# Kernel optimization log

Hardware: AMD Instinct MI355X
Metric: run time of the kernel (lower is better)

Reference implementation:

```python
import jax, jax.numpy as jnp
import numpy as np

EMBED = 1024
HEADS = 16
HEAD_DIM = EMBED // HEADS
MLP_DIM = 4096
EPS = 1e-5


def setup_inputs() -> dict:
    key = jax.random.key(0)
    ks = jax.random.split(key, 12)
    s = lambda d: 1.0 / np.sqrt(d)
    return {
        "x": jax.random.normal(ks[0], (8, 1024, EMBED), dtype=jnp.float32),
        "ln1_g": jnp.ones((EMBED,), jnp.float32),
        "ln1_b": jnp.zeros((EMBED,), jnp.float32),
        "w_qkv": jax.random.normal(ks[1], (EMBED, 3 * EMBED), jnp.float32) * s(EMBED),
        "b_qkv": jnp.zeros((3 * EMBED,), jnp.float32),
        "w_proj": jax.random.normal(ks[2], (EMBED, EMBED), jnp.float32) * s(EMBED),
        "b_proj": jnp.zeros((EMBED,), jnp.float32),
        "ln2_g": jnp.ones((EMBED,), jnp.float32),
        "ln2_b": jnp.zeros((EMBED,), jnp.float32),
        "w_fc1": jax.random.normal(ks[3], (EMBED, MLP_DIM), jnp.float32) * s(EMBED),
        "b_fc1": jnp.zeros((MLP_DIM,), jnp.float32),
        "w_fc2": jax.random.normal(ks[4], (MLP_DIM, EMBED), jnp.float32) * s(MLP_DIM),
        "b_fc2": jnp.zeros((EMBED,), jnp.float32),
    }


def _layernorm(x, g, b):
    mu = jnp.mean(x, axis=-1, keepdims=True)
    var = jnp.mean(jnp.square(x - mu), axis=-1, keepdims=True)
    return (x - mu) * jax.lax.rsqrt(var + EPS) * g + b


def reference(x, ln1_g, ln1_b, w_qkv, b_qkv, w_proj, b_proj,
              ln2_g, ln2_b, w_fc1, b_fc1, w_fc2, b_fc2):
    B, N, D = x.shape
    scale = HEAD_DIM ** -0.5

    # --- attention branch ---
    h = _layernorm(x, ln1_g, ln1_b)
    qkv = h @ w_qkv + b_qkv                       # [B,N,3D]
    qkv = qkv.reshape(B, N, 3, HEADS, HEAD_DIM)
    q, k, v = jnp.moveaxis(qkv, 2, 0)             # each [B,N,H,hd]
    attn = jnp.einsum('bqhd,bkhd->bhqk', q, k) * scale
    attn = jax.nn.softmax(attn, axis=-1)
    out = jnp.einsum('bhqk,bkhd->bqhd', attn, v).reshape(B, N, D)
    x = x + (out @ w_proj + b_proj)

    # --- MLP branch ---
    h = _layernorm(x, ln2_g, ln2_b)
    h = jax.nn.gelu(h @ w_fc1 + b_fc1, approximate=False)
    x = x + (h @ w_fc2 + b_fc2)
    return x
```

## Files before the change

kernel.cpp:

```cpp
#include <hip/hip_runtime.h>
#include <cstdint>


typedef unsigned short u16;
typedef short short8 __attribute__((ext_vector_type(8)));
typedef float floatx4 __attribute__((ext_vector_type(4)));

#define GLB(p) ((const __attribute__((address_space(1))) void*)(p))
#define LDSP(p) ((__attribute__((address_space(3))) void*)(p))

__device__ __forceinline__ u16 f2bf(float f) {
    uint32_t u = __float_as_uint(f);
    u += 0x7fffu + ((u >> 16) & 1u);
    return (u16)(u >> 16);
}
__device__ __forceinline__ uint32_t pack2(float a, float b) {
    return (uint32_t)f2bf(a) | ((uint32_t)f2bf(b) << 16);
}
__device__ __forceinline__ float fast_gelu(float v) {
    float u = v * (0.7978845608f + 0.0356774081f * v * v);
    float e = __expf(2.0f * u);
    float th = 1.0f - 2.0f * __builtin_amdgcn_rcpf(e + 1.0f);
    return 0.5f * v * (1.0f + th);
}

__global__ __launch_bounds__(256) void transpose_cast_kernel(
    const float* __restrict__ W, u16* __restrict__ Wt, int K, int N)
{
    __shared__ float tile[32][33];
    int n0 = blockIdx.x * 32, k0 = blockIdx.y * 32;
    int tx = threadIdx.x, ty = threadIdx.y;
    #pragma unroll
    for (int i = 0; i < 4; ++i)
        tile[ty + i * 8][tx] = W[(size_t)(k0 + ty + i * 8) * N + n0 + tx];
    __syncthreads();
    #pragma unroll
    for (int i = 0; i < 4; ++i)
        Wt[(size_t)(n0 + ty + i * 8) * K + k0 + tx] = f2bf(tile[tx][ty + i * 8]);
}

__global__ __launch_bounds__(256) void ln_kernel(
    const float* __restrict__ x, const float* __restrict__ gw,
    const float* __restrict__ bw, u16* __restrict__ out)
{
    const int row = blockIdx.x, tid = threadIdx.x;
    float4 v = ((const float4*)(x + (size_t)row * 1024))[tid];
    float s  = v.x + v.y + v.z + v.w;
    float ss = v.x * v.x + v.y * v.y + v.z * v.z + v.w * v.w;
    #pragma unroll
    for (int off = 32; off > 0; off >>= 1) {
        s  += __shfl_down(s, off);
        ss += __shfl_down(ss, off);
    }
    __shared__ float red[8];
    if ((tid & 63) == 0) { red[tid >> 6] = s; red[4 + (tid >> 6)] = ss; }
    __syncthreads();
    float S  = red[0] + red[1] + red[2] + red[3];
    float SS = red[4] + red[5] + red[6] + red[7];
    float mu  = S * (1.0f / 1024.0f);
    float var = SS * (1.0f / 1024.0f) - mu * mu;
    float rs  = rsqrtf(var + 1e-5f);
    float4 g4 = ((const float4*)gw)[tid];
    float4 b4 = ((const float4*)bw)[tid];
    u16* o = out + (size_t)row * 1024 + tid * 4;
    o[0] = f2bf((v.x - mu) * rs * g4.x + b4.x);
    o[1] = f2bf((v.y - mu) * rs * g4.y + b4.y);
    o[2] = f2bf((v.z - mu) * rs * g4.z + b4.z);
    o[3] = f2bf((v.w - mu) * rs * g4.w + b4.w);
}

__global__ __launch_bounds__(256) void add2_kernel(
    const float* __restrict__ a, const float* __restrict__ b,
    float* __restrict__ o, int n4)
{
    int i = blockIdx.x * 256 + threadIdx.x;
    const int stride = gridDim.x * 256;
    for (; i < n4; i += stride) {
        float4 va = ((const float4*)a)[i], vb = ((const float4*)b)[i];
        ((float4*)o)[i] = make_float4(va.x + vb.x, va.y + vb.y, va.z + vb.z, va.w + vb.w);
    }
}

#define MODE_BF16      0
#define MODE_BF16_GELU 1
#define MODE_F32_RES   2
#define MODE_QKV       3
#define MODE_F32_SPLIT 4

#define G8_BUF1 32768
#define G8_LDS_BYTES 131072

#define SB()    __builtin_amdgcn_sched_barrier(0)
#define BARR()  do { __builtin_amdgcn_s_barrier(); SB(); } while (0)
#define GATE4() do { asm volatile("s_waitcnt vmcnt(4)" ::: "memory"); SB(); } while (0)
#define WL0()   do { asm volatile("s_waitcnt lgkmcnt(0)" ::: "memory"); SB(); } while (0)

#define RDA(DST, BUFOFF, MH) \
    _Pragma("unroll") \
    for (int mt = 0; mt < 4; ++mt) \
        _Pragma("unroll") \
        for (int ks = 0; ks < 2; ++ks) \
            DST[mt][ks] = *(const short8*)&lds[(BUFOFF) + \
                (size_t)(wr * 128 + (MH) * 64 + mt * 16 + lc) * 64 + \
                (((ks * 4 + lg) ^ (lc & 7)) * 8)];

#define RDB(DST, BUFOFF, NH) \
    _Pragma("unroll") \
    for (int nn = 0; nn < 2; ++nn) \
        _Pragma("unroll") \
        for (int ks = 0; ks < 2; ++ks) \
            DST[nn][ks] = *(const short8*)&lds[(BUFOFF) + 16384 + \
                (size_t)(wc * 64 + (NH) * 32 + nn * 16 + lc) * 64 + \
                (((ks * 4 + lg) ^ (lc & 7)) * 8)];

#define MMAQ(MH, NH, FA, FB) \
    __builtin_amdgcn_s_setprio(1); \
    _Pragma("unroll") \
    for (int ks = 0; ks < 2; ++ks) \
        _Pragma("unroll") \
        for (int mt = 0; mt < 4; ++mt) \
            _Pragma("unroll") \
            for (int nn = 0; nn < 2; ++nn) \
                acc[(MH) * 4 + mt][(NH) * 2 + nn] = \
                    __builtin_amdgcn_mfma_f32_16x16x32_bf16( \
                        FA[mt][ks], FB[nn][ks], acc[(MH) * 4 + mt][(NH) * 2 + nn], 0, 0, 0); \
    __builtin_amdgcn_s_setprio(0);

template<int MODE>
__global__ __launch_bounds__(512, 2) void gemm8_kernel(
    const u16* __restrict__ A, const u16* __restrict__ Bt,
    const float* __restrict__ bias, const float* __restrict__ res,
    void* __restrict__ outv, u16* __restrict__ vt,
    int M, int N, int lda, int ldb, int K)
{
    extern __shared__ u16 lds[];
    const int tid = threadIdx.x;
    const int wave = tid >> 6, lane = tid & 63;
    const int lg = lane >> 4, lc = lane & 15;
    const int m0 = blockIdx.y * 256, n0 = blockIdx.x * 256;
    const int wr = wave >> 2, wc = wave & 3;
    const int zed = (MODE == MODE_F32_SPLIT) ? blockIdx.z : 0;
    if (MODE == MODE_F32_SPLIT && zed) { A += K; Bt += K; }

    floatx4 acc[8][4];
    #pragma unroll
    for (int i = 0; i < 8; ++i)
        #pragma unroll
        for (int j = 0; j < 4; ++j) acc[i][j] = floatx4{0.f, 0.f, 0.f, 0.f};

    const int srow = lane >> 3;
    const int schunk = (lane & 7) ^ srow;

    const u16* Abase = A  + (size_t)(m0 + wave * 8 + srow) * lda + schunk * 8;
    const u16* Bbase = Bt + (size_t)(n0 + wave * 8 + srow) * ldb + schunk * 8;

    auto stageH = [&](int b, int o, int h, int kk) {
        if (o == 0) {
            const u16* src = Abase + (size_t)h * 128 * lda + kk;
            u16* dst = lds + b * G8_BUF1 + h * 8192 + wave * 512;
            __builtin_amdgcn_global_load_lds(GLB(src), LDSP(dst), 16, 0, 0);
            __builtin_amdgcn_global_load_lds(GLB(src + (size_t)64 * lda), LDSP(dst + 4096), 16, 0, 0);
        } else {
            const u16* src = Bbase + (size_t)h * 128 * ldb + kk;
            u16* dst = lds + b * G8_BUF1 + 16384 + h * 8192 + wave * 512;
            __builtin_amdgcn_global_load_lds(GLB(src), LDSP(dst), 16, 0, 0);
            __builtin_amdgcn_global_load_lds(GLB(src + (size_t)64 * ldb), LDSP(dst + 4096), 16, 0, 0);
        }
    };

    const int nt = K >> 6;

    stageH(0, 0, 0, 0); stageH(0, 0, 1, 0); stageH(0, 1, 0, 0); stageH(0, 1, 1, 0);
    stageH(1, 0, 0, 64);

    short8 fa0[4][2], fa1[4][2], fb0[2][2], fb1[2][2];

    for (int t0 = 0; t0 < nt; t0 += 2) {
        const int kk1 = (t0 + 1) * 64;
        const int kk2 = ((t0 + 2 < nt) ? t0 + 2 : nt - 1) * 64;
        const int kk3 = ((t0 + 3 < nt) ? t0 + 3 : nt - 1) * 64;
        stageH(1, 0, 1, kk1); GATE4(); BARR();
        RDA(fa0, 0, 0) RDB(fb0, 0, 0) WL0();
        MMAQ(0, 0, fa0, fb0)
        stageH(1, 1, 0, kk1); BARR();
        RDA(fa1, 0, 1) WL0();
        MMAQ(1, 0, fa1, fb0)
        stageH(1, 1, 1, kk1); BARR();
        RDB(fb1, 0, 1) WL0();
        MMAQ(1, 1, fa1, fb1)
        stageH(0, 0, 0, kk2); BARR();
        MMAQ(0, 1, fa0, fb1)
        stageH(0, 0, 1, kk2); GATE4(); BARR();
        RDA(fa0, G8_BUF1, 0) RDB(fb0, G8_BUF1, 0) WL0();
        MMAQ(0, 0, fa0, fb0)
        stageH(0, 1, 0, kk2); BARR();
        RDA(fa1, G8_BUF1, 1) WL0();
        MMAQ(1, 0, fa1, fb0)
        stageH(0, 1, 1, kk2); BARR();
        RDB(fb1, G8_BUF1, 1) WL0();
        MMAQ(1, 1, fa1, fb1)
        stageH(1, 0, 0, kk3); BARR();
        MMAQ(0, 1, fa0, fb1)
    }

    if (MODE == MODE_QKV && n0 >= 2048) {
        #pragma unroll
        for (int mt = 0; mt < 8; ++mt) {
            #pragma unroll
            for (int nn = 0; nn < 4; ++nn) {
                const int col = n0 + wc * 64 + nn * 16 + lc;
                const float bv = bias[col];
                const int hd = col - 2048;
                const int rowbase = m0 + wr * 128 + mt * 16 + lg * 4;
                const int b = rowbase >> 10, token = rowbase & 1023;
                float v0 = acc[mt][nn][0] + bv, v1 = acc[mt][nn][1] + bv;
                float v2 = acc[mt][nn][2] + bv, v3 = acc[mt][nn][3] + bv;
                uint2 pk = {pack2(v0, v1), pack2(v2, v3)};
                *(uint2*)&vt[((size_t)b * 1024 + hd) * 1024 + token] = pk;
            }
        }
        return;
    }
    float* osel = (MODE == MODE_F32_SPLIT && zed) ? (float*)vt : (float*)outv;
    #pragma unroll
    for (int mt = 0; mt < 8; ++mt) {
        #pragma unroll
        for (int nn = 0; nn < 4; ++nn) {
            const int col = n0 + wc * 64 + nn * 16 + lc;
            const float bv = (MODE == MODE_F32_SPLIT && zed) ? 0.f : bias[col];
            #pragma unroll
            for (int r = 0; r < 4; ++r) {
                const int row = m0 + wr * 128 + mt * 16 + lg * 4 + r;
                float v = acc[mt][nn][r] + bv;
                if (MODE == MODE_BF16 || MODE == MODE_QKV) {
                    ((u16*)outv)[(size_t)row * N + col] = f2bf(v);
                } else if (MODE == MODE_BF16_GELU) {
                    ((u16*)outv)[(size_t)row * N + col] = f2bf(fast_gelu(v));
                } else if (MODE == MODE_F32_RES) {
                    ((float*)outv)[(size_t)row * N + col] = v + res[(size_t)row * N + col];
                } else {
                    osel[(size_t)row * N + col] = zed ? v : (v + res[(size_t)row * N + col]);
                }
            }
        }
    }
}

__global__ __launch_bounds__(256) void attn_kernel(
    const u16* __restrict__ qkv, const u16* __restrict__ vtg, u16* __restrict__ out)
{
    const int bid = blockIdx.x;
    const int g = ((bid >> 7) << 3) | (bid & 7);
    const int qt = (bid >> 3) & 15;
    const int h = g & 15, b = g >> 4;
    const int tid = threadIdx.x, wave = tid >> 6, lane = tid & 63;
    const int lg = lane >> 4, lc = lane & 15;

    __shared__ __attribute__((aligned(16))) u16 Qs[64 * 64];
    __shared__ __attribute__((aligned(16))) u16 Ks[64 * 64];
    __shared__ __attribute__((aligned(16))) u16 Vts[64 * 64];
    __shared__ __attribute__((aligned(16))) u16 Ps[64 * 64];

    const int q0 = qt * 64;
    const size_t hb = ((size_t)b * 1024) * 3072 + h * 64;
    const u16* vhead = vtg + ((size_t)b * 1024 + h * 64) * 1024;
    const int srow = lane >> 3;
    const int schunk = (lane & 7) ^ srow;

    {
        const u16* Qg = qkv + hb + (size_t)(q0 + wave * 16 + srow) * 3072 + schunk * 8;
        u16* Qw = &Qs[wave * 1024];
        __builtin_amdgcn_global_load_lds(GLB(Qg), LDSP(Qw), 16, 0, 0);
        __builtin_amdgcn_global_load_lds(GLB(Qg + (size_t)8 * 3072), LDSP(Qw + 512), 16, 0, 0);
    }
    __syncthreads();
    short8 aq[2];
    aq[0] = *(const short8*)&Qs[(wave * 16 + lc) * 64 + (((0 + lg) ^ (lc & 7)) * 8)];
    aq[1] = *(const short8*)&Qs[(wave * 16 + lc) * 64 + (((4 + lg) ^ (lc & 7)) * 8)];

    floatx4 o[4];
    #pragma unroll
    for (int dt = 0; dt < 4; ++dt) o[dt] = floatx4{0.f, 0.f, 0.f, 0.f};
    float mprev = -INFINITY, lsum = 0.f;
    const float sc = 0.125f;

    for (int kt = 0; kt < 16; ++kt) {
        __syncthreads();
        {
            const u16* Kg = qkv + hb + 1024 +
                (size_t)(kt * 64 + wave * 16 + srow) * 3072 + schunk * 8;
            u16* Kw = &Ks[wave * 1024];
            __builtin_amdgcn_global_load_lds(GLB(Kg), LDSP(Kw), 16, 0, 0);
            __builtin_amdgcn_global_load_lds(GLB(Kg + (size_t)8 * 3072), LDSP(Kw + 512), 16, 0, 0);
        }
        {
            const u16* Vg = vhead + (size_t)(wave * 16 + srow) * 1024 + kt * 64 + schunk * 8;
            u16* Vw = &Vts[wave * 1024];
            __builtin_amdgcn_global_load_lds(GLB(Vg), LDSP(Vw), 16, 0, 0);
            __builtin_amdgcn_global_load_lds(GLB(Vg + (size_t)8 * 1024), LDSP(Vw + 512), 16, 0, 0);
        }
        __syncthreads();

        floatx4 st[4];
        #pragma unroll
        for (int nt = 0; nt < 4; ++nt) st[nt] = floatx4{0.f, 0.f, 0.f, 0.f};
        #pragma unroll
        for (int ks = 0; ks < 2; ++ks)
            #pragma unroll
            for (int nt = 0; nt < 4; ++nt) {
                short8 fk = *(const short8*)&Ks[(nt * 16 + lc) * 64 +
                                                (((ks * 4 + lg) ^ (lc & 7)) * 8)];
                st[nt] = __builtin_amdgcn_mfma_f32_16x16x32_bf16(fk, aq[ks], st[nt], 0, 0, 0);
            }

        float m = st[0][0];
        #pragma unroll
        for (int nt = 0; nt < 4; ++nt)
            #pragma unroll
            for (int r = 0; r < 4; ++r) m = fmaxf(m, st[nt][r]);
        m = fmaxf(m, __shfl_xor(m, 16));
        m = fmaxf(m, __shfl_xor(m, 32));
        float mn = fmaxf(mprev, m * sc);
        float aexp = __expf(mprev - mn);
        mprev = mn;

        const int q = wave * 16 + lc;
        float rs = 0.f;
        #pragma unroll
        for (int nt = 0; nt < 4; ++nt) {
            float p0 = __expf(st[nt][0] * sc - mn);
            float p1 = __expf(st[nt][1] * sc - mn);
            float p2 = __expf(st[nt][2] * sc - mn);
            float p3 = __expf(st[nt][3] * sc - mn);
            rs += (p0 + p1) + (p2 + p3);
            const int c16 = nt * 2 + (lg >> 1);
            uint2 pk = {pack2(p0, p1), pack2(p2, p3)};
            *(uint2*)&Ps[q * 64 + ((c16 ^ (lc & 7)) * 8) + (lg & 1) * 4] = pk;
        }
        rs += __shfl_xor(rs, 16);
        rs += __shfl_xor(rs, 32);
        lsum = lsum * aexp + rs;
        #pragma unroll
        for (int dt = 0; dt < 4; ++dt)
            #pragma unroll
            for (int r = 0; r < 4; ++r) o[dt][r] *= aexp;

        #pragma unroll
        for (int ks = 0; ks < 2; ++ks) {
            short8 fp = *(const short8*)&Ps[q * 64 + (((ks * 4 + lg) ^ (lc & 7)) * 8)];
            #pragma unroll
            for (int dt = 0; dt < 4; ++dt) {
                short8 fv = *(const short8*)&Vts[(dt * 16 + lc) * 64 +
                                                 (((ks * 4 + lg) ^ (lc & 7)) * 8)];
                o[dt] = __builtin_amdgcn_mfma_f32_16x16x32_bf16(fv, fp, o[dt], 0, 0, 0);
            }
        }
    }

    const float rl = 1.0f / lsum;
    const int q = q0 + wave * 16 + lc;
    #pragma unroll
    for (int dt = 0; dt < 4; ++dt) {
        uint2 pk = {pack2(o[dt][0] * rl, o[dt][1] * rl),
                    pack2(o[dt][2] * rl, o[dt][3] * rl)};
        *(uint2*)&out[((size_t)b * 1024 + q) * 1024 + h * 64 + dt * 16 + lg * 4] = pk;
    }
}

extern "C" void kernel_launch(void* const* d_in, const int* in_sizes, int n_in,
                              void* d_out, int out_size, void* d_ws, size_t ws_size,
                              hipStream_t stream)
{
    const float* x      = (const float*)d_in[0];
    const float* ln1_g  = (const float*)d_in[1];
    const float* ln1_b  = (const float*)d_in[2];
    const float* w_qkv  = (const float*)d_in[3];
    const float* b_qkv  = (const float*)d_in[4];
    const float* w_proj = (const float*)d_in[5];
    const float* b_proj = (const float*)d_in[6];
    const float* ln2_g  = (const float*)d_in[7];
    const float* ln2_b  = (const float*)d_in[8];
    const float* w_fc1  = (const float*)d_in[9];
    const float* b_fc1  = (const float*)d_in[10];
    const float* w_fc2  = (const float*)d_in[11];
    const float* b_fc2  = (const float*)d_in[12];
    float* outp = (float*)d_out;

    char* ws = (char*)d_ws;
    size_t off = 0;
    auto alloc = [&](size_t bytes) { void* p = ws + off; off += (bytes + 255) & ~(size_t)255; return p; };
    u16*  wqkvT  = (u16*)alloc((size_t)3072 * 1024 * 2);
    u16*  wprojT = (u16*)alloc((size_t)1024 * 1024 * 2);
    u16*  wfc1T  = (u16*)alloc((size_t)4096 * 1024 * 2);
    u16*  hbuf   = (u16*)alloc((size_t)8192 * 1024 * 2);
    u16*  wfc2T  = (u16*)alloc((size_t)1024 * 4096 * 2);
    u16*  big    = (u16*)alloc((size_t)8192 * 4096 * 2);
    u16*  vtbuf  = (u16*)alloc((size_t)8 * 1024 * 1024 * 2);
    u16*  attno  = (u16*)alloc((size_t)8192 * 1024 * 2);
    float* x2    = (float*)alloc((size_t)8192 * 1024 * 4);
    float* p0    = (float*)vtbuf;
    float* p1    = (float*)wqkvT;

    static bool attr_done = []{
        hipFuncSetAttribute(reinterpret_cast<const void*>(gemm8_kernel<MODE_QKV>),
                            hipFuncAttributeMaxDynamicSharedMemorySize, G8_LDS_BYTES);
        hipFuncSetAttribute(reinterpret_cast<const void*>(gemm8_kernel<MODE_BF16_GELU>),
                            hipFuncAttributeMaxDynamicSharedMemorySize, G8_LDS_BYTES);
        hipFuncSetAttribute(reinterpret_cast<const void*>(gemm8_kernel<MODE_F32_RES>),
                            hipFuncAttributeMaxDynamicSharedMemorySize, G8_LDS_BYTES);
        hipFuncSetAttribute(reinterpret_cast<const void*>(gemm8_kernel<MODE_F32_SPLIT>),
                            hipFuncAttributeMaxDynamicSharedMemorySize, G8_LDS_BYTES);
        return true;
    }();
    (void)attr_done;

    dim3 tb(32, 8);
    transpose_cast_kernel<<<dim3(3072 / 32, 1024 / 32), tb, 0, stream>>>(w_qkv,  wqkvT,  1024, 3072);
    transpose_cast_kernel<<<dim3(1024 / 32, 1024 / 32), tb, 0, stream>>>(w_proj, wprojT, 1024, 1024);
    transpose_cast_kernel<<<dim3(4096 / 32, 1024 / 32), tb, 0, stream>>>(w_fc1,  wfc1T,  1024, 4096);
    transpose_cast_kernel<<<dim3(1024 / 32, 4096 / 32), tb, 0, stream>>>(w_fc2,  wfc2T,  4096, 1024);

    ln_kernel<<<8192, 256, 0, stream>>>(x, ln1_g, ln1_b, hbuf);
    gemm8_kernel<MODE_QKV><<<dim3(3072 / 256, 8192 / 256), 512, G8_LDS_BYTES, stream>>>(
        hbuf, wqkvT, b_qkv, nullptr, big, vtbuf, 8192, 3072, 1024, 1024, 1024);
    attn_kernel<<<2048, 256, 0, stream>>>(big, vtbuf, attno);
    gemm8_kernel<MODE_F32_RES><<<dim3(1024 / 256, 8192 / 256), 512, G8_LDS_BYTES, stream>>>(
        attno, wprojT, b_proj, x, x2, nullptr, 8192, 1024, 1024, 1024, 1024);
    ln_kernel<<<8192, 256, 0, stream>>>(x2, ln2_g, ln2_b, hbuf);
    gemm8_kernel<MODE_BF16_GELU><<<dim3(4096 / 256, 8192 / 256), 512, G8_LDS_BYTES, stream>>>(
        hbuf, wfc1T, b_fc1, nullptr, big, nullptr, 8192, 4096, 1024, 1024, 1024);
    gemm8_kernel<MODE_F32_SPLIT><<<dim3(1024 / 256, 8192 / 256, 2), 512, G8_LDS_BYTES, stream>>>(
        big, wfc2T, b_fc2, x2, p0, (u16*)p1, 8192, 1024, 4096, 4096, 2048);
    add2_kernel<<<2048, 256, 0, stream>>>(p0, p1, outp, 8192 * 1024 / 4);
}
```

Baseline: 507.1 us.

## Restructure GEMM pipeline waits and remap workgroups for XCD locality

Reorders the double-buffered GEMM main loop so LDS fragment reads are issued before each barrier, and moves the vmcnt gate to the ends of half-iterations with a tighter count. It also rebalances one stage load between half-steps and drains outstanding loads before the epilogue. Separately, it remaps linear workgroup IDs so consecutive tiles land on the same XCD chiplet, aiming at better L2 reuse. The reordered waits risk data races if the gating counts do not match the stages still in flight.

```diff
diff --git a/kernel.cpp b/kernel.cpp
--- a/kernel.cpp
+++ b/kernel.cpp
@@ -92,7 +92,7 @@
 
 #define SB()    __builtin_amdgcn_sched_barrier(0)
 #define BARR()  do { __builtin_amdgcn_s_barrier(); SB(); } while (0)
-#define GATE4() do { asm volatile("s_waitcnt vmcnt(4)" ::: "memory"); SB(); } while (0)
+#define GATE2() do { asm volatile("s_waitcnt vmcnt(2)" ::: "memory"); SB(); } while (0)
 #define WL0()   do { asm volatile("s_waitcnt lgkmcnt(0)" ::: "memory"); SB(); } while (0)
 
 #define RDA(DST, BUFOFF, MH) \
@@ -137,7 +137,11 @@
     const int tid = threadIdx.x;
     const int wave = tid >> 6, lane = tid & 63;
     const int lg = lane >> 4, lc = lane & 15;
-    const int m0 = blockIdx.y * 256, n0 = blockIdx.x * 256;
+    const int nx = gridDim.x, nwg = nx * gridDim.y;
+    const int orig = blockIdx.y * nx + blockIdx.x;
+    const int q = nwg >> 3, r = nwg & 7, xc = orig & 7, oo = orig >> 3;
+    const int sid = (xc < r ? xc * (q + 1) : r * (q + 1) + (xc - r) * q) + oo;
+    const int m0 = (sid / nx) * 256, n0 = (sid % nx) * 256;
     const int wr = wave >> 2, wc = wave & 3;
     const int zed = (MODE == MODE_F32_SPLIT) ? blockIdx.z : 0;
     if (MODE == MODE_F32_SPLIT && zed) { A += K; Bt += K; }
@@ -172,6 +176,7 @@
 
     stageH(0, 0, 0, 0); stageH(0, 0, 1, 0); stageH(0, 1, 0, 0); stageH(0, 1, 1, 0);
     stageH(1, 0, 0, 64);
+    GATE2(); BARR();
 
     short8 fa0[4][2], fa1[4][2], fb0[2][2], fb1[2][2];
 
@@ -179,29 +184,37 @@
         const int kk1 = (t0 + 1) * 64;
         const int kk2 = ((t0 + 2 < nt) ? t0 + 2 : nt - 1) * 64;
         const int kk3 = ((t0 + 3 < nt) ? t0 + 3 : nt - 1) * 64;
-        stageH(1, 0, 1, kk1); GATE4(); BARR();
-        RDA(fa0, 0, 0) RDB(fb0, 0, 0) WL0();
+        stageH(1, 0, 1, kk1);
+        RDA(fa0, 0, 0) RDB(fb0, 0, 0) SB();
+        BARR(); WL0();
         MMAQ(0, 0, fa0, fb0)
-        stageH(1, 1, 0, kk1); BARR();
-        RDA(fa1, 0, 1) WL0();
+        stageH(1, 1, 0, kk1);
+        RDA(fa1, 0, 1) SB();
+        BARR(); WL0();
         MMAQ(1, 0, fa1, fb0)
-        stageH(1, 1, 1, kk1); BARR();
-        RDB(fb1, 0, 1) WL0();
+        stageH(1, 1, 1, kk1);
+        RDB(fb1, 0, 1) SB();
+        BARR(); WL0();
         MMAQ(1, 1, fa1, fb1)
-        stageH(0, 0, 0, kk2); BARR();
+        stageH(0, 0, 0, kk2); GATE2();
+        BARR();
         MMAQ(0, 1, fa0, fb1)
-        stageH(0, 0, 1, kk2); GATE4(); BARR();
-        RDA(fa0, G8_BUF1, 0) RDB(fb0, G8_BUF1, 0) WL0();
+        stageH(0, 0, 1, kk2); stageH(0, 1, 0, kk2);
+        RDA(fa0, G8_BUF1, 0) RDB(fb0, G8_BUF1, 0) SB();
+        BARR(); WL0();
         MMAQ(0, 0, fa0, fb0)
-        stageH(0, 1, 0, kk2); BARR();
-        RDA(fa1, G8_BUF1, 1) WL0();
+        stageH(0, 1, 1, kk2);
+        RDA(fa1, G8_BUF1, 1) SB();
+        BARR(); WL0();
         MMAQ(1, 0, fa1, fb0)
-        stageH(0, 1, 1, kk2); BARR();
-        RDB(fb1, G8_BUF1, 1) WL0();
+        RDB(fb1, G8_BUF1, 1) SB();
+        BARR(); WL0();
         MMAQ(1, 1, fa1, fb1)
-        stageH(1, 0, 0, kk3); BARR();
+        stageH(1, 0, 0, kk3); GATE2();
+        BARR();
         MMAQ(0, 1, fa0, fb1)
     }
+    asm volatile("s_waitcnt vmcnt(0)" ::: "memory");
 
     if (MODE == MODE_QKV && n0 >= 2048) {
         #pragma unroll
```

Result: no change. 500.5 us (-1.3%).
